# Kernel optimization log

Measured on AMD Instinct MI355X. Metric: run time of the kernel, lower is better.

## Reference

```python
import jax, jax.numpy as jnp
import numpy as np

N_NODES = 50000
N_EDGES = 1600000
D_IN = 128
D_HID = 128
D_OUT = 128


def setup_inputs() -> dict:
    key = jax.random.key(0)
    k1, k2, k3, k4, k5, k6 = jax.random.split(key, 6)
    x = jax.random.normal(k1, (N_NODES, D_IN), dtype=jnp.float32)
    edge_index = jax.random.randint(k2, (2, N_EDGES), 0, N_NODES, dtype=jnp.int64)
    # glorot-ish init for GCNConv linear weights; bias zeros-like but randomized small
    W1 = jax.random.normal(k3, (D_IN, D_HID), dtype=jnp.float32) * (1.0 / np.sqrt(D_IN))
    b1 = jax.random.normal(k4, (D_HID,), dtype=jnp.float32) * 0.01
    W2 = jax.random.normal(k5, (D_HID, D_OUT), dtype=jnp.float32) * (1.0 / np.sqrt(D_HID))
    b2 = jax.random.normal(k6, (D_OUT,), dtype=jnp.float32) * 0.01
    return {"x": x, "edge_index": edge_index, "W1": W1, "b1": b1, "W2": W2, "b2": b2}


def gcn_conv(x, src, dst, W, b, n_nodes):
    # PyG GCNConv: add self-loops, symmetric normalization deg^-1/2, lin -> aggregate -> +bias
    loop = jnp.arange(n_nodes, dtype=src.dtype)
    s = jnp.concatenate([src, loop])  # [E+N]
    d = jnp.concatenate([dst, loop])  # [E+N]
    deg = jax.ops.segment_sum(jnp.ones_like(d, dtype=x.dtype), d, num_segments=n_nodes)
    dinv = jnp.where(deg > 0, jax.lax.rsqrt(deg), 0.0)
    norm = dinv[s] * dinv[d]  # [E+N]
    h = x @ W  # [N, F_out]
    msg = h[s] * norm[:, None]  # gather + scale: [E+N, F_out]
    out = jax.ops.segment_sum(msg, d, num_segments=n_nodes)  # scatter-add
    return out + b


def reference(x, edge_index, W1, b1, W2, b2):
    src, dst = edge_index[0], edge_index[1]
    h = gcn_conv(x, src, dst, W1, b1, N_NODES)
    h = jnp.where(h >= 0, h, 0.1 * h)  # LeakyReLU(0.1)
    h = gcn_conv(h, src, dst, W2, b2, N_NODES)
    return h.mean(axis=1)  # [N]
```

## Files before the change

kernel.cpp:

```cpp
#include <hip/hip_runtime.h>
#include <hip/hip_bf16.h>


#define N_NODES 50000
#define NPAD 50048
#define D 128
#define BK 196
#define CHUNK 4096

typedef unsigned int uint;
typedef unsigned short u16;
typedef __attribute__((ext_vector_type(8))) short short8;
typedef __attribute__((ext_vector_type(4))) float floatx4;

__device__ __forceinline__ u16 cvt_bf16(float f) {
    uint u = __float_as_uint(f);
    return (u16)((u + 0x7fffu + ((u >> 16) & 1u)) >> 16);
}
__device__ __forceinline__ uint pack_bf2(float a, float b) {
    return (uint)cvt_bf16(a) | ((uint)cvt_bf16(b) << 16);
}

__global__ void hist_w2m_kernel(const int* __restrict__ dst, uint* __restrict__ H,
                                const float* __restrict__ W2, const float* __restrict__ b2,
                                float* __restrict__ w2m, uint* __restrict__ counter,
                                int E, int CHN) {
    int t = threadIdx.x, c = blockIdx.x;
    if (c < CHN) {
        __shared__ uint h[BK];
        if (t < BK) h[t] = 0;
        __syncthreads();
        int e0 = c * CHUNK;
        for (int i = t; i < CHUNK; i += 256) {
            int e = e0 + i;
            if (e < E) atomicAdd(&h[dst[e] >> 8], 1u);
        }
        __syncthreads();
        if (t < BK) H[t * CHN + c] = h[t];
    } else {
        if (t < 128) {
            float s = 0.f;
            for (int j = 0; j < 128; j++) s += W2[t * 128 + j];
            w2m[t] = s * (1.0f / 128.0f);
        } else if (t == 128) {
            float s = 0.f;
            for (int j = 0; j < 128; j++) s += b2[j];
            w2m[128] = s * (1.0f / 128.0f);
        } else if (t == 129) {
            *counter = 0;
        }
    }
}

__global__ void scan_kernel(uint* __restrict__ H, uint* __restrict__ T, uint* __restrict__ B,
                            int* __restrict__ row, uint* __restrict__ counter,
                            int CHN, int E, int N) {
    __shared__ uint s[256];
    __shared__ uint ticket_sh;
    int t = threadIdx.x, b = blockIdx.x;
    uint carry = 0;
    for (int base = 0; base < CHN; base += 256) {
        int idx = base + t;
        uint v = (idx < CHN) ? H[b * CHN + idx] : 0u;
        s[t] = v;
        __syncthreads();
#pragma unroll
        for (int off = 1; off < 256; off <<= 1) {
            uint u = (t >= off) ? s[t - off] : 0u;
            __syncthreads();
            s[t] += u;
            __syncthreads();
        }
        if (idx < CHN) H[b * CHN + idx] = carry + s[t] - v;
        carry += s[255];
        __syncthreads();
    }
    if (t == 0) {
        atomicExch(&T[b], carry);
        __threadfence();
        ticket_sh = atomicAdd(counter, 1);
    }
    __syncthreads();
    if (ticket_sh == (uint)(gridDim.x - 1)) {
        __threadfence();
        uint v = (t < BK) ? atomicAdd(&T[t], 0u) : 0u;
        s[t] = v;
        __syncthreads();
#pragma unroll
        for (int off = 1; off < 256; off <<= 1) {
            uint u = (t >= off) ? s[t - off] : 0u;
            __syncthreads();
            s[t] += u;
            __syncthreads();
        }
        if (t < BK) B[t] = s[t] - v;
        if (t == 0) { B[BK] = (uint)E; row[N] = E; }
    }
}

__global__ void scatter_kernel(const int* __restrict__ src, const int* __restrict__ dst,
                               const uint* __restrict__ H, const uint* __restrict__ B,
                               uint* __restrict__ EB, int E, int CHN) {
    __shared__ uint cur[BK];
    int t = threadIdx.x, c = blockIdx.x;
    if (t < BK) cur[t] = B[t] + H[t * CHN + c];
    __syncthreads();
    int e0 = c * CHUNK;
    for (int i = t; i < CHUNK; i += 256) {
        int e = e0 + i;
        if (e < E) {
            int d = dst[e];
            uint slot = atomicAdd(&cur[d >> 8], 1u);
            EB[slot] = ((uint)(d & 255) << 16) | (uint)src[e];
        }
    }
}

#define WT_STRIDE 136
union SortGemmSmem {
    struct { uint cnt[256], s[256], cur[256]; } sort;
    u16 wt[128 * WT_STRIDE];
};
__global__ __launch_bounds__(256) void sortgemm_kernel(
    const uint* __restrict__ EB, const uint* __restrict__ B,
    int* __restrict__ row, float* __restrict__ dinv, u16* __restrict__ esrc,
    const float* __restrict__ A, const float* __restrict__ W,
    uint* __restrict__ G32, int N, int M) {
    __shared__ SortGemmSmem sm;
    int t = threadIdx.x;

    if (blockIdx.x < BK) {
        int b = blockIdx.x;
        uint base = B[b], ne = B[b + 1] - base;
        sm.sort.cnt[t] = 0;
        __syncthreads();
        for (uint i = t; i < ne; i += 256) atomicAdd(&sm.sort.cnt[EB[base + i] >> 16], 1u);
        __syncthreads();
        uint c = sm.sort.cnt[t];
        sm.sort.s[t] = c;
        __syncthreads();
#pragma unroll
        for (int off = 1; off < 256; off <<= 1) {
            uint u = (t >= off) ? sm.sort.s[t - off] : 0u;
            __syncthreads();
            sm.sort.s[t] += u;
            __syncthreads();
        }
        uint p = sm.sort.s[t] - c;
        int v = (b << 8) + t;
        if (v < N) {
            row[v] = (int)(base + p);
            dinv[v] = rsqrtf((float)(c + 1u));
        }
        sm.sort.cur[t] = base + p;
        __syncthreads();
        for (uint i = t; i < ne; i += 256) {
            uint u = EB[base + i];
            uint slot = atomicAdd(&sm.sort.cur[u >> 16], 1u);
            esrc[slot] = (u16)(u & 0xffffu);
        }
    } else {
        int bid = blockIdx.x - BK;
        for (int i = t; i < 128 * 128; i += 256) {
            int k = i >> 7, n = i & 127;
            sm.wt[n * WT_STRIDE + k] = cvt_bf16(W[i]);
        }
        __syncthreads();

        int wave = t >> 6, lane = t & 63;
        int m = lane & 15, quad = lane >> 4;
        int rowa = bid * 64 + wave * 16 + m;
        int rowc = rowa < M ? rowa : M - 1;
        const float* Arow = A + (long)rowc * D;

        short8 afrag[4];
#pragma unroll
        for (int kt = 0; kt < 4; kt++) {
            int k0 = kt * 32 + quad * 8;
            float4 f0 = *(const float4*)(Arow + k0);
            float4 f1 = *(const float4*)(Arow + k0 + 4);
            short8 af;
            af[0] = (short)cvt_bf16(f0.x); af[1] = (short)cvt_bf16(f0.y);
            af[2] = (short)cvt_bf16(f0.z); af[3] = (short)cvt_bf16(f0.w);
            af[4] = (short)cvt_bf16(f1.x); af[5] = (short)cvt_bf16(f1.y);
            af[6] = (short)cvt_bf16(f1.z); af[7] = (short)cvt_bf16(f1.w);
            afrag[kt] = af;
        }

        int orow0 = bid * 64 + wave * 16;
        for (int n0 = 0; n0 < 128; n0 += 16) {
            floatx4 acc = {0.f, 0.f, 0.f, 0.f};
#pragma unroll
            for (int kt = 0; kt < 4; kt++) {
                short8 bf = *(const short8*)(sm.wt + (n0 + m) * WT_STRIDE + kt * 32 + quad * 8);
                acc = __builtin_amdgcn_mfma_f32_16x16x32_bf16(afrag[kt], bf, acc, 0, 0, 0);
            }
#pragma unroll
            for (int r = 0; r < 4; r++) {
                float val = acc[r];
                float oth = __shfl_xor(val, 1, 64);
                int orow = orow0 + quad * 4 + r;
                if (orow < M && (m & 1) == 0)
                    G32[(long)orow * 64 + ((n0 + m) >> 1)] = pack_bf2(val, oth);
            }
        }
    }
}

__global__ __launch_bounds__(256) void gather_node_kernel(
    const int* __restrict__ row, const u16* __restrict__ esrc,
    const uint* __restrict__ g16, const float* __restrict__ dinv,
    const float* __restrict__ b1, const float* __restrict__ w2m,
    float* __restrict__ mg, int N) {
    int wave = threadIdx.x >> 6;
    int lane = threadIdx.x & 63;
    int sub = lane & 7;
    int nb = lane >> 3;
    int v = blockIdx.x * 4 + wave;
    if (v >= N) return;

    const uint4* gv = (const uint4*)g16;
    float dvv = dinv[v];
    float acc[16];
#pragma unroll
    for (int i = 0; i < 16; i++) acc[i] = 0.f;

#define ACC8(ua, ub, wgt) {                                              \
    uint uu[8] = {(ua).x, (ua).y, (ua).z, (ua).w, (ub).x, (ub).y, (ub).z, (ub).w}; \
    _Pragma("unroll")                                                    \
    for (int i = 0; i < 8; i++) {                                        \
        acc[2*i]   += (wgt) * __uint_as_float(uu[i] << 16);              \
        acc[2*i+1] += (wgt) * __uint_as_float(uu[i] & 0xffff0000u);      \
    } }

    if (nb == 0) {
        long rb = (long)v * 16 + 2 * sub;
        uint4 ua = gv[rb], ub = gv[rb + 1];
        ACC8(ua, ub, dvv)
    }
    int jb = row[v], je = row[v + 1];
    int j = jb + nb;
    if (j < je) {
        int s0 = esrc[j];
        float wA = dinv[s0];
        long r0 = (long)s0 * 16 + 2 * sub;
        uint4 p0 = gv[r0], p1 = gv[r0 + 1];
        j += 8;
        while (j < je) {
            int s1 = esrc[j];
            float wB = dinv[s1];
            long r1 = (long)s1 * 16 + 2 * sub;
            uint4 q0 = gv[r1], q1 = gv[r1 + 1];
            j += 8;
            ACC8(p0, p1, wA)
            p0 = q0; p1 = q1; wA = wB;
        }
        ACC8(p0, p1, wA)
    }
#undef ACC8

#pragma unroll
    for (int i = 0; i < 16; i++) {
        acc[i] += __shfl_xor(acc[i], 8, 64);
        acc[i] += __shfl_xor(acc[i], 16, 64);
        acc[i] += __shfl_xor(acc[i], 32, 64);
    }

    if (nb == 0) {
        const float4* bp = (const float4*)b1;
        const float4* wp = (const float4*)w2m;
        float s = 0.f;
#pragma unroll
        for (int q4 = 0; q4 < 4; q4++) {
            float4 bb = bp[sub * 4 + q4];
            float4 wm = wp[sub * 4 + q4];
            float t0 = dvv * acc[4*q4 + 0] + bb.x; t0 = t0 >= 0.f ? t0 : 0.1f * t0;
            float t1 = dvv * acc[4*q4 + 1] + bb.y; t1 = t1 >= 0.f ? t1 : 0.1f * t1;
            float t2 = dvv * acc[4*q4 + 2] + bb.z; t2 = t2 >= 0.f ? t2 : 0.1f * t2;
            float t3 = dvv * acc[4*q4 + 3] + bb.w; t3 = t3 >= 0.f ? t3 : 0.1f * t3;
            s += t0 * wm.x + t1 * wm.y + t2 * wm.z + t3 * wm.w;
        }
        s += __shfl_xor(s, 1, 64);
        s += __shfl_xor(s, 2, 64);
        s += __shfl_xor(s, 4, 64);
        if (sub == 0) mg[v] = dvv * s;
    }
}

__global__ void out_kernel(const int* __restrict__ row, const u16* __restrict__ esrc,
                           const float* __restrict__ mg, const float* __restrict__ dinv,
                           const float* __restrict__ w2m, float* __restrict__ out, int N) {
    int v = blockIdx.x * blockDim.x + threadIdx.x;
    if (v >= N) return;
    float acc = mg[v];
    int jb = row[v], je = row[v + 1];
    int j = jb;
    for (; j + 8 <= je; j += 8) {
        acc += mg[esrc[j]] + mg[esrc[j + 1]] + mg[esrc[j + 2]] + mg[esrc[j + 3]] +
               mg[esrc[j + 4]] + mg[esrc[j + 5]] + mg[esrc[j + 6]] + mg[esrc[j + 7]];
    }
    for (; j < je; j++) acc += mg[esrc[j]];
    out[v] = dinv[v] * acc + w2m[128];
}

extern "C" void kernel_launch(void* const* d_in, const int* in_sizes, int n_in,
                              void* d_out, int out_size, void* d_ws, size_t ws_size,
                              hipStream_t stream) {
    const float* x  = (const float*)d_in[0];
    const int* ei   = (const int*)d_in[1];
    const float* W1 = (const float*)d_in[2];
    const float* b1 = (const float*)d_in[3];
    const float* W2 = (const float*)d_in[4];
    const float* b2 = (const float*)d_in[5];
    float* out = (float*)d_out;

    const int N = N_NODES;
    const int E = in_sizes[1] / 2;
    const int* src = ei;
    const int* dst = ei + E;
    const int CHN = (E + CHUNK - 1) / CHUNK;
    const int nblocks = (N + 255) / 256;

    float*    dinv    = (float*)d_ws;
    int*      row     = (int*)(dinv + NPAD);
    uint*     B       = (uint*)(row + NPAD + 16);
    float*    w2m     = (float*)(B + 256);
    float*    mg      = w2m + 256;
    uint*     T       = (uint*)(mg + NPAD);
    uint*     counter = T + 256;
    uint*     g16u    = counter + 16;
    u16*      esrc    = (u16*)(g16u + (long)NPAD * 64);
    uint*     H       = (uint*)(esrc + E);
    uint*     EB      = H + BK * CHN;

    hist_w2m_kernel<<<CHN + 1, 256, 0, stream>>>(dst, H, W2, b2, w2m, counter, E, CHN);
    scan_kernel<<<BK, 256, 0, stream>>>(H, T, B, row, counter, CHN, E, N);
    scatter_kernel<<<CHN, 256, 0, stream>>>(src, dst, H, B, EB, E, CHN);
    sortgemm_kernel<<<BK + (N + 63) / 64, 256, 0, stream>>>(EB, B, row, dinv, esrc,
                                                            x, W1, g16u, N, N);
    gather_node_kernel<<<(N + 3) / 4, 256, 0, stream>>>(row, esrc, g16u, dinv, b1, w2m, mg, N);
    out_kernel<<<nblocks, 256, 0, stream>>>(row, esrc, mg, dinv, w2m, out, N);
}
```

Baseline: 197.8 us.

## Merge six kernels into three using cooperative grid syncs

Collapses the pipeline from six launches to three. The GEMM moves into the histogram kernel so it can overlap with counting. Scan, scatter and per-bucket sort become one cooperative kernel separated by grid.sync, and the gather and output passes become one persistent cooperative kernel. The aim is to cut launch gaps and tail idle time between small stages, at the cost of grid-wide barriers, a persistent loop with capped occupancy, and a dependence on cooperative launch limits (grid sizes 391 and up to 2048 blocks).

```diff
diff --git a/kernel.cpp b/kernel.cpp
--- a/kernel.cpp
+++ b/kernel.cpp
@@ -1,5 +1,8 @@
 #include <hip/hip_runtime.h>
 #include <hip/hip_bf16.h>
+#include <hip/hip_cooperative_groups.h>
+
+namespace cg = cooperative_groups;
 
 
 #define N_NODES 50000
@@ -7,6 +10,7 @@
 #define D 128
 #define BK 196
 #define CHUNK 4096
+#define WT_STRIDE 136
 
 typedef unsigned int uint;
 typedef unsigned short u16;
@@ -21,23 +25,29 @@
     return (uint)cvt_bf16(a) | ((uint)cvt_bf16(b) << 16);
 }
 
-__global__ void hist_w2m_kernel(const int* __restrict__ dst, uint* __restrict__ H,
-                                const float* __restrict__ W2, const float* __restrict__ b2,
-                                float* __restrict__ w2m, uint* __restrict__ counter,
-                                int E, int CHN) {
+__global__ __launch_bounds__(256) void hist_w2m_gemm_kernel(
+    const int* __restrict__ dst, uint* __restrict__ H,
+    const float* __restrict__ W2, const float* __restrict__ b2,
+    float* __restrict__ w2m,
+    const float* __restrict__ A, const float* __restrict__ W,
+    uint* __restrict__ G32, int E, int CHN, int N) {
+    __shared__ union {
+        uint h[BK];
+        u16 wt[128 * WT_STRIDE];
+    } sm;
     int t = threadIdx.x, c = blockIdx.x;
+
     if (c < CHN) {
-        __shared__ uint h[BK];
-        if (t < BK) h[t] = 0;
+        if (t < BK) sm.h[t] = 0;
         __syncthreads();
         int e0 = c * CHUNK;
         for (int i = t; i < CHUNK; i += 256) {
             int e = e0 + i;
-            if (e < E) atomicAdd(&h[dst[e] >> 8], 1u);
-        }
-        __syncthreads();
-        if (t < BK) H[t * CHN + c] = h[t];
-    } else {
+            if (e < E) atomicAdd(&sm.h[dst[e] >> 8], 1u);
+        }
+        __syncthreads();
+        if (t < BK) H[t * CHN + c] = sm.h[t];
+    } else if (c == CHN) {
         if (t < 128) {
             float s = 0.f;
             for (int j = 0; j < 128; j++) s += W2[t * 128 + j];
@@ -46,121 +56,9 @@
             float s = 0.f;
             for (int j = 0; j < 128; j++) s += b2[j];
             w2m[128] = s * (1.0f / 128.0f);
-        } else if (t == 129) {
-            *counter = 0;
-        }
-    }
-}
-
-__global__ void scan_kernel(uint* __restrict__ H, uint* __restrict__ T, uint* __restrict__ B,
-                            int* __restrict__ row, uint* __restrict__ counter,
-                            int CHN, int E, int N) {
-    __shared__ uint s[256];
-    __shared__ uint ticket_sh;
-    int t = threadIdx.x, b = blockIdx.x;
-    uint carry = 0;
-    for (int base = 0; base < CHN; base += 256) {
-        int idx = base + t;
-        uint v = (idx < CHN) ? H[b * CHN + idx] : 0u;
-        s[t] = v;
-        __syncthreads();
-#pragma unroll
-        for (int off = 1; off < 256; off <<= 1) {
-            uint u = (t >= off) ? s[t - off] : 0u;
-            __syncthreads();
-            s[t] += u;
-            __syncthreads();
-        }
-        if (idx < CHN) H[b * CHN + idx] = carry + s[t] - v;
-        carry += s[255];
-        __syncthreads();
-    }
-    if (t == 0) {
-        atomicExch(&T[b], carry);
-        __threadfence();
-        ticket_sh = atomicAdd(counter, 1);
-    }
-    __syncthreads();
-    if (ticket_sh == (uint)(gridDim.x - 1)) {
-        __threadfence();
-        uint v = (t < BK) ? atomicAdd(&T[t], 0u) : 0u;
-        s[t] = v;
-        __syncthreads();
-#pragma unroll
-        for (int off = 1; off < 256; off <<= 1) {
-            uint u = (t >= off) ? s[t - off] : 0u;
-            __syncthreads();
-            s[t] += u;
-            __syncthreads();
-        }
-        if (t < BK) B[t] = s[t] - v;
-        if (t == 0) { B[BK] = (uint)E; row[N] = E; }
-    }
-}
-
-__global__ void scatter_kernel(const int* __restrict__ src, const int* __restrict__ dst,
-                               const uint* __restrict__ H, const uint* __restrict__ B,
-                               uint* __restrict__ EB, int E, int CHN) {
-    __shared__ uint cur[BK];
-    int t = threadIdx.x, c = blockIdx.x;
-    if (t < BK) cur[t] = B[t] + H[t * CHN + c];
-    __syncthreads();
-    int e0 = c * CHUNK;
-    for (int i = t; i < CHUNK; i += 256) {
-        int e = e0 + i;
-        if (e < E) {
-            int d = dst[e];
-            uint slot = atomicAdd(&cur[d >> 8], 1u);
-            EB[slot] = ((uint)(d & 255) << 16) | (uint)src[e];
-        }
-    }
-}
-
-#define WT_STRIDE 136
-union SortGemmSmem {
-    struct { uint cnt[256], s[256], cur[256]; } sort;
-    u16 wt[128 * WT_STRIDE];
-};
-__global__ __launch_bounds__(256) void sortgemm_kernel(
-    const uint* __restrict__ EB, const uint* __restrict__ B,
-    int* __restrict__ row, float* __restrict__ dinv, u16* __restrict__ esrc,
-    const float* __restrict__ A, const float* __restrict__ W,
-    uint* __restrict__ G32, int N, int M) {
-    __shared__ SortGemmSmem sm;
-    int t = threadIdx.x;
-
-    if (blockIdx.x < BK) {
-        int b = blockIdx.x;
-        uint base = B[b], ne = B[b + 1] - base;
-        sm.sort.cnt[t] = 0;
-        __syncthreads();
-        for (uint i = t; i < ne; i += 256) atomicAdd(&sm.sort.cnt[EB[base + i] >> 16], 1u);
-        __syncthreads();
-        uint c = sm.sort.cnt[t];
-        sm.sort.s[t] = c;
-        __syncthreads();
-#pragma unroll
-        for (int off = 1; off < 256; off <<= 1) {
-            uint u = (t >= off) ? sm.sort.s[t - off] : 0u;
-            __syncthreads();
-            sm.sort.s[t] += u;
-            __syncthreads();
-        }
-        uint p = sm.sort.s[t] - c;
-        int v = (b << 8) + t;
-        if (v < N) {
-            row[v] = (int)(base + p);
-            dinv[v] = rsqrtf((float)(c + 1u));
-        }
-        sm.sort.cur[t] = base + p;
-        __syncthreads();
-        for (uint i = t; i < ne; i += 256) {
-            uint u = EB[base + i];
-            uint slot = atomicAdd(&sm.sort.cur[u >> 16], 1u);
-            esrc[slot] = (u16)(u & 0xffffu);
         }
     } else {
-        int bid = blockIdx.x - BK;
+        int bid = c - CHN - 1;
         for (int i = t; i < 128 * 128; i += 256) {
             int k = i >> 7, n = i & 127;
             sm.wt[n * WT_STRIDE + k] = cvt_bf16(W[i]);
@@ -170,7 +68,7 @@
         int wave = t >> 6, lane = t & 63;
         int m = lane & 15, quad = lane >> 4;
         int rowa = bid * 64 + wave * 16 + m;
-        int rowc = rowa < M ? rowa : M - 1;
+        int rowc = rowa < N ? rowa : N - 1;
         const float* Arow = A + (long)rowc * D;
 
         short8 afrag[4];
@@ -200,30 +98,122 @@
                 float val = acc[r];
                 float oth = __shfl_xor(val, 1, 64);
                 int orow = orow0 + quad * 4 + r;
-                if (orow < M && (m & 1) == 0)
+                if (orow < N && (m & 1) == 0)
                     G32[(long)orow * 64 + ((n0 + m) >> 1)] = pack_bf2(val, oth);
             }
         }
     }
 }
 
-__global__ __launch_bounds__(256) void gather_node_kernel(
+__global__ __launch_bounds__(256) void build_kernel(
+    const int* __restrict__ src, const int* __restrict__ dst,
+    uint* __restrict__ H, uint* __restrict__ T, uint* __restrict__ B,
+    int* __restrict__ row, float* __restrict__ dinv, u16* __restrict__ esrc,
+    uint* __restrict__ EB, int E, int N, int CHN) {
+    cg::grid_group grid = cg::this_grid();
+    __shared__ union {
+        uint s[256];
+        struct { uint cnt[256]; uint s2[256]; uint cur2[256]; } srt;
+        uint cur[BK];
+    } sm;
+    int t = threadIdx.x, b = blockIdx.x;
+
+    if (b < BK) {
+        uint carry = 0;
+        for (int base = 0; base < CHN; base += 256) {
+            int idx = base + t;
+            uint v = (idx < CHN) ? H[b * CHN + idx] : 0u;
+            sm.s[t] = v;
+            __syncthreads();
+#pragma unroll
+            for (int off = 1; off < 256; off <<= 1) {
+                uint u = (t >= off) ? sm.s[t - off] : 0u;
+                __syncthreads();
+                sm.s[t] += u;
+                __syncthreads();
+            }
+            if (idx < CHN) H[b * CHN + idx] = carry + sm.s[t] - v;
+            carry += sm.s[255];
+            __syncthreads();
+        }
+        if (t == 0) atomicExch(&T[b], carry);
+    }
+    grid.sync();
+
+    if (b == 0) {
+        uint v = (t < BK) ? atomicAdd(&T[t], 0u) : 0u;
+        sm.s[t] = v;
+        __syncthreads();
+#pragma unroll
+        for (int off = 1; off < 256; off <<= 1) {
+            uint u = (t >= off) ? sm.s[t - off] : 0u;
+            __syncthreads();
+            sm.s[t] += u;
+            __syncthreads();
+        }
+        if (t < BK) B[t] = sm.s[t] - v;
+        if (t == 0) { B[BK] = (uint)E; row[N] = E; }
+    }
+    grid.sync();
+
+    if (b < CHN) {
+        if (t < BK) sm.cur[t] = B[t] + H[t * CHN + b];
+        __syncthreads();
+        int e0 = b * CHUNK;
+        for (int i = t; i < CHUNK; i += 256) {
+            int e = e0 + i;
+            if (e < E) {
+                int d = dst[e];
+                uint slot = atomicAdd(&sm.cur[d >> 8], 1u);
+                EB[slot] = ((uint)(d & 255) << 16) | (uint)src[e];
+            }
+        }
+    }
+    grid.sync();
+
+    if (b < BK) {
+        uint base = B[b], ne = B[b + 1] - base;
+        sm.srt.cnt[t] = 0;
+        __syncthreads();
+        for (uint i = t; i < ne; i += 256) atomicAdd(&sm.srt.cnt[EB[base + i] >> 16], 1u);
+        __syncthreads();
+        uint cval = sm.srt.cnt[t];
+        sm.srt.s2[t] = cval;
+        __syncthreads();
+#pragma unroll
+        for (int off = 1; off < 256; off <<= 1) {
+            uint u = (t >= off) ? sm.srt.s2[t - off] : 0u;
+            __syncthreads();
+            sm.srt.s2[t] += u;
+            __syncthreads();
+        }
+        uint p = sm.srt.s2[t] - cval;
+        int v = (b << 8) + t;
+        if (v < N) {
+            row[v] = (int)(base + p);
+            dinv[v] = rsqrtf((float)(cval + 1u));
+        }
+        sm.srt.cur2[t] = base + p;
+        __syncthreads();
+        for (uint i = t; i < ne; i += 256) {
+            uint u = EB[base + i];
+            uint slot = atomicAdd(&sm.srt.cur2[u >> 16], 1u);
+            esrc[slot] = (u16)(u & 0xffffu);
+        }
+    }
+}
+
+__global__ __launch_bounds__(256, 8) void gather_out_kernel(
     const int* __restrict__ row, const u16* __restrict__ esrc,
     const uint* __restrict__ g16, const float* __restrict__ dinv,
     const float* __restrict__ b1, const float* __restrict__ w2m,
-    float* __restrict__ mg, int N) {
+    float* __restrict__ mg, float* __restrict__ out, int N) {
+    cg::grid_group grid = cg::this_grid();
     int wave = threadIdx.x >> 6;
     int lane = threadIdx.x & 63;
     int sub = lane & 7;
     int nb = lane >> 3;
-    int v = blockIdx.x * 4 + wave;
-    if (v >= N) return;
-
     const uint4* gv = (const uint4*)g16;
-    float dvv = dinv[v];
-    float acc[16];
-#pragma unroll
-    for (int i = 0; i < 16; i++) acc[i] = 0.f;
 
 #define ACC8(ua, ub, wgt) {                                              \
     uint uu[8] = {(ua).x, (ua).y, (ua).z, (ua).w, (ub).x, (ub).y, (ub).z, (ub).w}; \
@@ -233,74 +223,83 @@
         acc[2*i+1] += (wgt) * __uint_as_float(uu[i] & 0xffff0000u);      \
     } }
 
-    if (nb == 0) {
-        long rb = (long)v * 16 + 2 * sub;
-        uint4 ua = gv[rb], ub = gv[rb + 1];
-        ACC8(ua, ub, dvv)
-    }
-    int jb = row[v], je = row[v + 1];
-    int j = jb + nb;
-    if (j < je) {
-        int s0 = esrc[j];
-        float wA = dinv[s0];
-        long r0 = (long)s0 * 16 + 2 * sub;
-        uint4 p0 = gv[r0], p1 = gv[r0 + 1];
-        j += 8;
-        while (j < je) {
-            int s1 = esrc[j];
-            float wB = dinv[s1];
-            long r1 = (long)s1 * 16 + 2 * sub;
-            uint4 q0 = gv[r1], q1 = gv[r1 + 1];
-            j += 8;
-            ACC8(p0, p1, wA)
-            p0 = q0; p1 = q1; wA = wB;
-        }
-        ACC8(p0, p1, wA)
+    for (int v0 = blockIdx.x * 4; v0 < N; v0 += gridDim.x * 4) {
+        int v = v0 + wave;
+        if (v < N) {
+            float dvv = dinv[v];
+            float acc[16];
+#pragma unroll
+            for (int i = 0; i < 16; i++) acc[i] = 0.f;
+
+            if (nb == 0) {
+                long rb = (long)v * 16 + 2 * sub;
+                uint4 ua = gv[rb], ub = gv[rb + 1];
+                ACC8(ua, ub, dvv)
+            }
+            int jb = row[v], je = row[v + 1];
+            int j = jb + nb;
+            if (j < je) {
+                int s0 = esrc[j];
+                float wA = dinv[s0];
+                long r0 = (long)s0 * 16 + 2 * sub;
+                uint4 p0 = gv[r0], p1 = gv[r0 + 1];
+                j += 8;
+                while (j < je) {
+                    int s1 = esrc[j];
+                    float wB = dinv[s1];
+                    long r1 = (long)s1 * 16 + 2 * sub;
+                    uint4 q0 = gv[r1], q1 = gv[r1 + 1];
+                    j += 8;
+                    ACC8(p0, p1, wA)
+                    p0 = q0; p1 = q1; wA = wB;
+                }
+                ACC8(p0, p1, wA)
+            }
+
+#pragma unroll
+            for (int i = 0; i < 16; i++) {
+                acc[i] += __shfl_xor(acc[i], 8, 64);
+                acc[i] += __shfl_xor(acc[i], 16, 64);
+                acc[i] += __shfl_xor(acc[i], 32, 64);
+            }
+
+            if (nb == 0) {
+                const float4* bp = (const float4*)b1;
+                const float4* wp = (const float4*)w2m;
+                float s = 0.f;
+#pragma unroll
+                for (int q4 = 0; q4 < 4; q4++) {
+                    float4 bb = bp[sub * 4 + q4];
+                    float4 wm = wp[sub * 4 + q4];
+                    float t0 = dvv * acc[4*q4 + 0] + bb.x; t0 = t0 >= 0.f ? t0 : 0.1f * t0;
+                    float t1 = dvv * acc[4*q4 + 1] + bb.y; t1 = t1 >= 0.f ? t1 : 0.1f * t1;
+                    float t2 = dvv * acc[4*q4 + 2] + bb.z; t2 = t2 >= 0.f ? t2 : 0.1f * t2;
+                    float t3 = dvv * acc[4*q4 + 3] + bb.w; t3 = t3 >= 0.f ? t3 : 0.1f * t3;
+                    s += t0 * wm.x + t1 * wm.y + t2 * wm.z + t3 * wm.w;
+                }
+                s += __shfl_xor(s, 1, 64);
+                s += __shfl_xor(s, 2, 64);
+                s += __shfl_xor(s, 4, 64);
+                if (sub == 0) mg[v] = dvv * s;
+            }
+        }
     }
 #undef ACC8
 
-#pragma unroll
-    for (int i = 0; i < 16; i++) {
-        acc[i] += __shfl_xor(acc[i], 8, 64);
-        acc[i] += __shfl_xor(acc[i], 16, 64);
-        acc[i] += __shfl_xor(acc[i], 32, 64);
-    }
-
-    if (nb == 0) {
-        const float4* bp = (const float4*)b1;
-        const float4* wp = (const float4*)w2m;
-        float s = 0.f;
-#pragma unroll
-        for (int q4 = 0; q4 < 4; q4++) {
-            float4 bb = bp[sub * 4 + q4];
-            float4 wm = wp[sub * 4 + q4];
-            float t0 = dvv * acc[4*q4 + 0] + bb.x; t0 = t0 >= 0.f ? t0 : 0.1f * t0;
-            float t1 = dvv * acc[4*q4 + 1] + bb.y; t1 = t1 >= 0.f ? t1 : 0.1f * t1;
-            float t2 = dvv * acc[4*q4 + 2] + bb.z; t2 = t2 >= 0.f ? t2 : 0.1f * t2;
-            float t3 = dvv * acc[4*q4 + 3] + bb.w; t3 = t3 >= 0.f ? t3 : 0.1f * t3;
-            s += t0 * wm.x + t1 * wm.y + t2 * wm.z + t3 * wm.w;
-        }
-        s += __shfl_xor(s, 1, 64);
-        s += __shfl_xor(s, 2, 64);
-        s += __shfl_xor(s, 4, 64);
-        if (sub == 0) mg[v] = dvv * s;
-    }
-}
-
-__global__ void out_kernel(const int* __restrict__ row, const u16* __restrict__ esrc,
-                           const float* __restrict__ mg, const float* __restrict__ dinv,
-                           const float* __restrict__ w2m, float* __restrict__ out, int N) {
-    int v = blockIdx.x * blockDim.x + threadIdx.x;
-    if (v >= N) return;
-    float acc = mg[v];
-    int jb = row[v], je = row[v + 1];
-    int j = jb;
-    for (; j + 8 <= je; j += 8) {
-        acc += mg[esrc[j]] + mg[esrc[j + 1]] + mg[esrc[j + 2]] + mg[esrc[j + 3]] +
-               mg[esrc[j + 4]] + mg[esrc[j + 5]] + mg[esrc[j + 6]] + mg[esrc[j + 7]];
-    }
-    for (; j < je; j++) acc += mg[esrc[j]];
-    out[v] = dinv[v] * acc + w2m[128];
+    grid.sync();
+
+    float w2c = w2m[128];
+    for (int v = blockIdx.x * 256 + threadIdx.x; v < N; v += gridDim.x * 256) {
+        float acc = mg[v];
+        int jb = row[v], je = row[v + 1];
+        int j = jb;
+        for (; j + 8 <= je; j += 8) {
+            acc += mg[esrc[j]] + mg[esrc[j + 1]] + mg[esrc[j + 2]] + mg[esrc[j + 3]] +
+                   mg[esrc[j + 4]] + mg[esrc[j + 5]] + mg[esrc[j + 6]] + mg[esrc[j + 7]];
+        }
+        for (; j < je; j++) acc += mg[esrc[j]];
+        out[v] = dinv[v] * acc + w2c;
+    }
 }
 
 extern "C" void kernel_launch(void* const* d_in, const int* in_sizes, int n_in,
@@ -314,12 +313,12 @@
     const float* b2 = (const float*)d_in[5];
     float* out = (float*)d_out;
 
-    const int N = N_NODES;
-    const int E = in_sizes[1] / 2;
+    int N = N_NODES;
+    int E = in_sizes[1] / 2;
     const int* src = ei;
     const int* dst = ei + E;
-    const int CHN = (E + CHUNK - 1) / CHUNK;
-    const int nblocks = (N + 255) / 256;
+    int CHN = (E + CHUNK - 1) / CHUNK;
+    int GB  = (N + 63) / 64;
 
     float*    dinv    = (float*)d_ws;
     int*      row     = (int*)(dinv + NPAD);
@@ -332,12 +331,36 @@
     u16*      esrc    = (u16*)(g16u + (long)NPAD * 64);
     uint*     H       = (uint*)(esrc + E);
     uint*     EB      = H + BK * CHN;
-
-    hist_w2m_kernel<<<CHN + 1, 256, 0, stream>>>(dst, H, W2, b2, w2m, counter, E, CHN);
-    scan_kernel<<<BK, 256, 0, stream>>>(H, T, B, row, counter, CHN, E, N);
-    scatter_kernel<<<CHN, 256, 0, stream>>>(src, dst, H, B, EB, E, CHN);
-    sortgemm_kernel<<<BK + (N + 63) / 64, 256, 0, stream>>>(EB, B, row, dinv, esrc,
-                                                            x, W1, g16u, N, N);
-    gather_node_kernel<<<(N + 3) / 4, 256, 0, stream>>>(row, esrc, g16u, dinv, b1, w2m, mg, N);
-    out_kernel<<<nblocks, 256, 0, stream>>>(row, esrc, mg, dinv, w2m, out, N);
-}
+    (void)counter;
+
+    hist_w2m_gemm_kernel<<<CHN + 1 + GB, 256, 0, stream>>>(dst, H, W2, b2, w2m,
+                                                           x, W1, g16u, E, CHN, N);
+
+    {
+        int grid2 = (CHN > BK) ? CHN : BK;
+        void* args[] = {(void*)&src, (void*)&dst, (void*)&H, (void*)&T, (void*)&B,
+                        (void*)&row, (void*)&dinv, (void*)&esrc, (void*)&EB,
+                        (void*)&E, (void*)&N, (void*)&CHN};
+        hipLaunchCooperativeKernel((const void*)build_kernel, dim3(grid2), dim3(256),
+                                   args, 0, stream);
+    }
+
+    {
+        static int maxb = -1;
+        if (maxb < 0) {
+            int mb = 0;
+            if (hipOccupancyMaxActiveBlocksPerMultiprocessor(
+                    &mb, (const void*)gather_out_kernel, 256, 0) != hipSuccess || mb < 1)
+                mb = 4;
+            maxb = mb;
+        }
+        int grid3 = maxb * 256;
+        int ng = (N + 3) / 4;
+        if (grid3 > ng) grid3 = ng;
+        if (grid3 > 2048) grid3 = 2048;
+        void* args[] = {(void*)&row, (void*)&esrc, (void*)&g16u, (void*)&dinv,
+                        (void*)&b1, (void*)&w2m, (void*)&mg, (void*)&out, (void*)&N};
+        hipLaunchCooperativeKernel((const void*)gather_out_kernel, dim3(grid3), dim3(256),
+                                   args, 0, stream);
+    }
+}
```

New measurement: 495.4 us. 2.5x slower.

## Replace two-level bucket sort with global-atomic degree count and fused scan

Applied to the files above, without the earlier changes.

Replaces the bucketed histogram, scan, scatter and local sort kernels with a per-node global atomic degree count, a scan that runs in the same launch and waits on spin counters, and a direct scatter via per-node global atomic cursors. This cuts the launch count from six to four plus a memset and removes the intermediate EB buffer and its second pass. The cost is heavy global atomic contention on 50k counters and inter-block spin waits, which can deadlock if the counting blocks are not scheduled before the waiting scan blocks. Edge order within a node also becomes nondeterministic.

```diff
diff --git a/kernel.cpp b/kernel.cpp
--- a/kernel.cpp
+++ b/kernel.cpp
@@ -5,8 +5,8 @@
 #define N_NODES 50000
 #define NPAD 50048
 #define D 128
-#define BK 196
 #define CHUNK 4096
+#define WT_STRIDE 136
 
 typedef unsigned int uint;
 typedef unsigned short u16;
@@ -21,23 +21,25 @@
     return (uint)cvt_bf16(a) | ((uint)cvt_bf16(b) << 16);
 }
 
-__global__ void hist_w2m_kernel(const int* __restrict__ dst, uint* __restrict__ H,
-                                const float* __restrict__ W2, const float* __restrict__ b2,
-                                float* __restrict__ w2m, uint* __restrict__ counter,
-                                int E, int CHN) {
+__global__ __launch_bounds__(256) void degscan_kernel(
+    const int* __restrict__ dst, const float* __restrict__ W2,
+    const float* __restrict__ b2, float* __restrict__ w2m,
+    int* __restrict__ row, uint* __restrict__ cnt, uint* __restrict__ T,
+    float* __restrict__ dinv, uint* __restrict__ cur,
+    int E, int CHN, int N) {
     int t = threadIdx.x, c = blockIdx.x;
+    uint* rowu = (uint*)row;
+
     if (c < CHN) {
-        __shared__ uint h[BK];
-        if (t < BK) h[t] = 0;
-        __syncthreads();
         int e0 = c * CHUNK;
         for (int i = t; i < CHUNK; i += 256) {
             int e = e0 + i;
-            if (e < E) atomicAdd(&h[dst[e] >> 8], 1u);
-        }
-        __syncthreads();
-        if (t < BK) H[t * CHN + c] = h[t];
-    } else {
+            if (e < E) atomicAdd(&rowu[dst[e]], 1u);
+        }
+        __threadfence();
+        __syncthreads();
+        if (t == 0) atomicAdd(&cnt[0], 1u);
+    } else if (c == CHN) {
         if (t < 128) {
             float s = 0.f;
             for (int j = 0; j < 128; j++) s += W2[t * 128 + j];
@@ -46,23 +48,19 @@
             float s = 0.f;
             for (int j = 0; j < 128; j++) s += b2[j];
             w2m[128] = s * (1.0f / 128.0f);
-        } else if (t == 129) {
-            *counter = 0;
-        }
-    }
-}
-
-__global__ void scan_kernel(uint* __restrict__ H, uint* __restrict__ T, uint* __restrict__ B,
-                            int* __restrict__ row, uint* __restrict__ counter,
-                            int CHN, int E, int N) {
-    __shared__ uint s[256];
-    __shared__ uint ticket_sh;
-    int t = threadIdx.x, b = blockIdx.x;
-    uint carry = 0;
-    for (int base = 0; base < CHN; base += 256) {
-        int idx = base + t;
-        uint v = (idx < CHN) ? H[b * CHN + idx] : 0u;
-        s[t] = v;
+        }
+    } else {
+        __shared__ uint s[256];
+        __shared__ uint Bb_sh;
+        int NSB = (int)gridDim.x - CHN - 1;
+        int b = c - CHN - 1;
+        if (t == 0) {
+            while (atomicAdd(&cnt[0], 0u) < (uint)CHN) __builtin_amdgcn_s_sleep(8);
+        }
+        __syncthreads();
+        int v = b * 256 + t;
+        uint cv = (v < N) ? atomicAdd(&rowu[v], 0u) : 0u;
+        s[t] = cv;
         __syncthreads();
 #pragma unroll
         for (int off = 1; off < 256; off <<= 1) {
@@ -71,20 +69,16 @@
             s[t] += u;
             __syncthreads();
         }
-        if (idx < CHN) H[b * CHN + idx] = carry + s[t] - v;
-        carry += s[255];
-        __syncthreads();
-    }
-    if (t == 0) {
-        atomicExch(&T[b], carry);
-        __threadfence();
-        ticket_sh = atomicAdd(counter, 1);
-    }
-    __syncthreads();
-    if (ticket_sh == (uint)(gridDim.x - 1)) {
-        __threadfence();
-        uint v = (t < BK) ? atomicAdd(&T[t], 0u) : 0u;
-        s[t] = v;
+        uint excl = s[t] - cv;
+        if (t == 0) {
+            atomicExch(&T[b], s[255]);
+            __threadfence();
+            atomicAdd(&cnt[1], 1u);
+            while (atomicAdd(&cnt[1], 0u) < (uint)NSB) __builtin_amdgcn_s_sleep(8);
+        }
+        __syncthreads();
+        uint tv = (t < NSB) ? atomicAdd(&T[t], 0u) : 0u;
+        s[t] = tv;
         __syncthreads();
 #pragma unroll
         for (int off = 1; off < 256; off <<= 1) {
@@ -93,77 +87,42 @@
             s[t] += u;
             __syncthreads();
         }
-        if (t < BK) B[t] = s[t] - v;
-        if (t == 0) { B[BK] = (uint)E; row[N] = E; }
-    }
-}
-
-__global__ void scatter_kernel(const int* __restrict__ src, const int* __restrict__ dst,
-                               const uint* __restrict__ H, const uint* __restrict__ B,
-                               uint* __restrict__ EB, int E, int CHN) {
-    __shared__ uint cur[BK];
-    int t = threadIdx.x, c = blockIdx.x;
-    if (t < BK) cur[t] = B[t] + H[t * CHN + c];
-    __syncthreads();
-    int e0 = c * CHUNK;
-    for (int i = t; i < CHUNK; i += 256) {
-        int e = e0 + i;
-        if (e < E) {
-            int d = dst[e];
-            uint slot = atomicAdd(&cur[d >> 8], 1u);
-            EB[slot] = ((uint)(d & 255) << 16) | (uint)src[e];
-        }
-    }
-}
-
-#define WT_STRIDE 136
-union SortGemmSmem {
-    struct { uint cnt[256], s[256], cur[256]; } sort;
-    u16 wt[128 * WT_STRIDE];
-};
-__global__ __launch_bounds__(256) void sortgemm_kernel(
-    const uint* __restrict__ EB, const uint* __restrict__ B,
-    int* __restrict__ row, float* __restrict__ dinv, u16* __restrict__ esrc,
+        if (t == b) Bb_sh = s[t] - tv;
+        __syncthreads();
+        uint base = Bb_sh;
+        if (v < N) {
+            uint r = base + excl;
+            row[v] = (int)r;
+            cur[v] = r;
+            dinv[v] = rsqrtf((float)(cv + 1u));
+        }
+        if (b == 0 && t == 0) row[N] = E;
+    }
+}
+
+__global__ __launch_bounds__(256) void scattergemm_kernel(
+    const int* __restrict__ src, const int* __restrict__ dst,
+    uint* __restrict__ cur, u16* __restrict__ esrc,
     const float* __restrict__ A, const float* __restrict__ W,
-    uint* __restrict__ G32, int N, int M) {
-    __shared__ SortGemmSmem sm;
+    uint* __restrict__ G32, int E, int CHN, int M) {
+    __shared__ u16 wt[128 * WT_STRIDE];
     int t = threadIdx.x;
 
-    if (blockIdx.x < BK) {
-        int b = blockIdx.x;
-        uint base = B[b], ne = B[b + 1] - base;
-        sm.sort.cnt[t] = 0;
-        __syncthreads();
-        for (uint i = t; i < ne; i += 256) atomicAdd(&sm.sort.cnt[EB[base + i] >> 16], 1u);
-        __syncthreads();
-        uint c = sm.sort.cnt[t];
-        sm.sort.s[t] = c;
-        __syncthreads();
-#pragma unroll
-        for (int off = 1; off < 256; off <<= 1) {
-            uint u = (t >= off) ? sm.sort.s[t - off] : 0u;
-            __syncthreads();
-            sm.sort.s[t] += u;
-            __syncthreads();
-        }
-        uint p = sm.sort.s[t] - c;
-        int v = (b << 8) + t;
-        if (v < N) {
-            row[v] = (int)(base + p);
-            dinv[v] = rsqrtf((float)(c + 1u));
-        }
-        sm.sort.cur[t] = base + p;
-        __syncthreads();
-        for (uint i = t; i < ne; i += 256) {
-            uint u = EB[base + i];
-            uint slot = atomicAdd(&sm.sort.cur[u >> 16], 1u);
-            esrc[slot] = (u16)(u & 0xffffu);
+    if (blockIdx.x < (uint)CHN) {
+        int e0 = blockIdx.x * CHUNK;
+        for (int i = t; i < CHUNK; i += 256) {
+            int e = e0 + i;
+            if (e < E) {
+                int d = dst[e];
+                uint slot = atomicAdd(&cur[d], 1u);
+                esrc[slot] = (u16)src[e];
+            }
         }
     } else {
-        int bid = blockIdx.x - BK;
+        int bid = blockIdx.x - CHN;
         for (int i = t; i < 128 * 128; i += 256) {
             int k = i >> 7, n = i & 127;
-            sm.wt[n * WT_STRIDE + k] = cvt_bf16(W[i]);
+            wt[n * WT_STRIDE + k] = cvt_bf16(W[i]);
         }
         __syncthreads();
 
@@ -192,7 +151,7 @@
             floatx4 acc = {0.f, 0.f, 0.f, 0.f};
 #pragma unroll
             for (int kt = 0; kt < 4; kt++) {
-                short8 bf = *(const short8*)(sm.wt + (n0 + m) * WT_STRIDE + kt * 32 + quad * 8);
+                short8 bf = *(const short8*)(wt + (n0 + m) * WT_STRIDE + kt * 32 + quad * 8);
                 acc = __builtin_amdgcn_mfma_f32_16x16x32_bf16(afrag[kt], bf, acc, 0, 0, 0);
             }
 #pragma unroll
@@ -319,25 +278,25 @@
     const int* src = ei;
     const int* dst = ei + E;
     const int CHN = (E + CHUNK - 1) / CHUNK;
-    const int nblocks = (N + 255) / 256;
-
-    float*    dinv    = (float*)d_ws;
-    int*      row     = (int*)(dinv + NPAD);
-    uint*     B       = (uint*)(row + NPAD + 16);
-    float*    w2m     = (float*)(B + 256);
-    float*    mg      = w2m + 256;
-    uint*     T       = (uint*)(mg + NPAD);
-    uint*     counter = T + 256;
-    uint*     g16u    = counter + 16;
-    u16*      esrc    = (u16*)(g16u + (long)NPAD * 64);
-    uint*     H       = (uint*)(esrc + E);
-    uint*     EB      = H + BK * CHN;
-
-    hist_w2m_kernel<<<CHN + 1, 256, 0, stream>>>(dst, H, W2, b2, w2m, counter, E, CHN);
-    scan_kernel<<<BK, 256, 0, stream>>>(H, T, B, row, counter, CHN, E, N);
-    scatter_kernel<<<CHN, 256, 0, stream>>>(src, dst, H, B, EB, E, CHN);
-    sortgemm_kernel<<<BK + (N + 63) / 64, 256, 0, stream>>>(EB, B, row, dinv, esrc,
-                                                            x, W1, g16u, N, N);
+    const int NSB = (N + 255) / 256;
+    const int GB  = (N + 63) / 64;
+
+    float*    dinv = (float*)d_ws;
+    int*      row  = (int*)(dinv + NPAD);
+    uint*     cnt  = (uint*)(row + NPAD);
+    uint*     T    = (uint*)(row + NPAD + 16);
+    float*    w2m  = (float*)(T + 256);
+    float*    mg   = w2m + 256;
+    uint*     cur  = (uint*)(mg + NPAD);
+    uint*     g16u = cur + NPAD;
+    u16*      esrc = (u16*)(g16u + (long)NPAD * 64);
+
+    hipMemsetAsync(row, 0, (size_t)(NPAD + 2) * sizeof(int), stream);
+
+    degscan_kernel<<<CHN + 1 + NSB, 256, 0, stream>>>(dst, W2, b2, w2m,
+                                                      row, cnt, T, dinv, cur, E, CHN, N);
+    scattergemm_kernel<<<CHN + GB, 256, 0, stream>>>(src, dst, cur, esrc,
+                                                     x, W1, g16u, E, CHN, N);
     gather_node_kernel<<<(N + 3) / 4, 256, 0, stream>>>(row, esrc, g16u, dinv, b1, w2m, mg, N);
-    out_kernel<<<nblocks, 256, 0, stream>>>(row, esrc, mg, dinv, w2m, out, N);
-}
+    out_kernel<<<NSB, 256, 0, stream>>>(row, esrc, mg, dinv, w2m, out, N);
+}
```

Measured after the change: 366.0 us. 1.85x slower.

## Batch neighbor index loads via wave shuffles and double GEMM rows per block

Applied to the files above, without the earlier changes.

The gather kernel now loads up to 64 neighbor indices and their dinv weights with one coalesced load per wave, then broadcasts them to the 8-lane subgroups with shuffles. This replaces the serial per-subgroup index and weight loads that sat on the dependent path. The fused GEMM branch now processes two 64-row groups per block, halving the GEMM block count and the cost of loading and converting W into shared memory. The trade-off is more shuffles and higher register pressure.

```diff
diff --git a/kernel.cpp b/kernel.cpp
--- a/kernel.cpp
+++ b/kernel.cpp
@@ -169,39 +169,43 @@
 
         int wave = t >> 6, lane = t & 63;
         int m = lane & 15, quad = lane >> 4;
-        int rowa = bid * 64 + wave * 16 + m;
-        int rowc = rowa < M ? rowa : M - 1;
-        const float* Arow = A + (long)rowc * D;
-
-        short8 afrag[4];
-#pragma unroll
-        for (int kt = 0; kt < 4; kt++) {
-            int k0 = kt * 32 + quad * 8;
-            float4 f0 = *(const float4*)(Arow + k0);
-            float4 f1 = *(const float4*)(Arow + k0 + 4);
-            short8 af;
-            af[0] = (short)cvt_bf16(f0.x); af[1] = (short)cvt_bf16(f0.y);
-            af[2] = (short)cvt_bf16(f0.z); af[3] = (short)cvt_bf16(f0.w);
-            af[4] = (short)cvt_bf16(f1.x); af[5] = (short)cvt_bf16(f1.y);
-            af[6] = (short)cvt_bf16(f1.z); af[7] = (short)cvt_bf16(f1.w);
-            afrag[kt] = af;
-        }
-
-        int orow0 = bid * 64 + wave * 16;
-        for (int n0 = 0; n0 < 128; n0 += 16) {
-            floatx4 acc = {0.f, 0.f, 0.f, 0.f};
+
+#pragma unroll
+        for (int rg = 0; rg < 2; rg++) {
+            int rowa = bid * 128 + rg * 64 + wave * 16 + m;
+            int rowc = rowa < M ? rowa : M - 1;
+            const float* Arow = A + (long)rowc * D;
+
+            short8 afrag[4];
 #pragma unroll
             for (int kt = 0; kt < 4; kt++) {
-                short8 bf = *(const short8*)(sm.wt + (n0 + m) * WT_STRIDE + kt * 32 + quad * 8);
-                acc = __builtin_amdgcn_mfma_f32_16x16x32_bf16(afrag[kt], bf, acc, 0, 0, 0);
+                int k0 = kt * 32 + quad * 8;
+                float4 f0 = *(const float4*)(Arow + k0);
+                float4 f1 = *(const float4*)(Arow + k0 + 4);
+                short8 af;
+                af[0] = (short)cvt_bf16(f0.x); af[1] = (short)cvt_bf16(f0.y);
+                af[2] = (short)cvt_bf16(f0.z); af[3] = (short)cvt_bf16(f0.w);
+                af[4] = (short)cvt_bf16(f1.x); af[5] = (short)cvt_bf16(f1.y);
+                af[6] = (short)cvt_bf16(f1.z); af[7] = (short)cvt_bf16(f1.w);
+                afrag[kt] = af;
             }
-#pragma unroll
-            for (int r = 0; r < 4; r++) {
-                float val = acc[r];
-                float oth = __shfl_xor(val, 1, 64);
-                int orow = orow0 + quad * 4 + r;
-                if (orow < M && (m & 1) == 0)
-                    G32[(long)orow * 64 + ((n0 + m) >> 1)] = pack_bf2(val, oth);
+
+            int orow0 = bid * 128 + rg * 64 + wave * 16;
+            for (int n0 = 0; n0 < 128; n0 += 16) {
+                floatx4 acc = {0.f, 0.f, 0.f, 0.f};
+#pragma unroll
+                for (int kt = 0; kt < 4; kt++) {
+                    short8 bf = *(const short8*)(sm.wt + (n0 + m) * WT_STRIDE + kt * 32 + quad * 8);
+                    acc = __builtin_amdgcn_mfma_f32_16x16x32_bf16(afrag[kt], bf, acc, 0, 0, 0);
+                }
+#pragma unroll
+                for (int r = 0; r < 4; r++) {
+                    float val = acc[r];
+                    float oth = __shfl_xor(val, 1, 64);
+                    int orow = orow0 + quad * 4 + r;
+                    if (orow < M && (m & 1) == 0)
+                        G32[(long)orow * 64 + ((n0 + m) >> 1)] = pack_bf2(val, oth);
+                }
             }
         }
     }
@@ -239,23 +243,46 @@
         ACC8(ua, ub, dvv)
     }
     int jb = row[v], je = row[v + 1];
-    int j = jb + nb;
-    if (j < je) {
-        int s0 = esrc[j];
-        float wA = dinv[s0];
-        long r0 = (long)s0 * 16 + 2 * sub;
-        uint4 p0 = gv[r0], p1 = gv[r0 + 1];
-        j += 8;
-        while (j < je) {
-            int s1 = esrc[j];
-            float wB = dinv[s1];
-            long r1 = (long)s1 * 16 + 2 * sub;
-            uint4 q0 = gv[r1], q1 = gv[r1 + 1];
-            j += 8;
+    for (int base = jb; base < je; base += 64) {
+        int navail = je - base; if (navail > 64) navail = 64;
+        int mi = 0; float mw = 0.f;
+        if (lane < navail) {
+            mi = (int)esrc[base + lane];
+            mw = dinv[mi];
+        }
+        int sk0, sk1, sk2, sk3, sk4, sk5, sk6, sk7;
+        float wk0, wk1, wk2, wk3, wk4, wk5, wk6, wk7;
+        sk0 = __shfl(mi, nb,      64); wk0 = __shfl(mw, nb,      64);
+        sk1 = __shfl(mi, nb + 8,  64); wk1 = __shfl(mw, nb + 8,  64);
+        sk2 = __shfl(mi, nb + 16, 64); wk2 = __shfl(mw, nb + 16, 64);
+        sk3 = __shfl(mi, nb + 24, 64); wk3 = __shfl(mw, nb + 24, 64);
+        sk4 = __shfl(mi, nb + 32, 64); wk4 = __shfl(mw, nb + 32, 64);
+        sk5 = __shfl(mi, nb + 40, 64); wk5 = __shfl(mw, nb + 40, 64);
+        sk6 = __shfl(mi, nb + 48, 64); wk6 = __shfl(mw, nb + 48, 64);
+        sk7 = __shfl(mi, nb + 56, 64); wk7 = __shfl(mw, nb + 56, 64);
+        int kmax = (navail > nb) ? ((navail - nb + 7) >> 3) : 0;
+
+        if (kmax > 0) {
+            long rA = (long)sk0 * 16 + 2 * sub;
+            uint4 p0 = gv[rA], p1 = gv[rA + 1];
+            float wA = wk0;
+#define SLOT(kk, skk, wkk) \
+            if (kk < kmax) { \
+                long rB = (long)(skk) * 16 + 2 * sub; \
+                uint4 q0 = gv[rB], q1 = gv[rB + 1]; \
+                ACC8(p0, p1, wA) \
+                p0 = q0; p1 = q1; wA = (wkk); \
+            }
+            SLOT(1, sk1, wk1)
+            SLOT(2, sk2, wk2)
+            SLOT(3, sk3, wk3)
+            SLOT(4, sk4, wk4)
+            SLOT(5, sk5, wk5)
+            SLOT(6, sk6, wk6)
+            SLOT(7, sk7, wk7)
+#undef SLOT
             ACC8(p0, p1, wA)
-            p0 = q0; p1 = q1; wA = wB;
-        }
-        ACC8(p0, p1, wA)
+        }
     }
 #undef ACC8
 
@@ -320,6 +347,7 @@
     const int* dst = ei + E;
     const int CHN = (E + CHUNK - 1) / CHUNK;
     const int nblocks = (N + 255) / 256;
+    const int GB = (N + 127) / 128;
 
     float*    dinv    = (float*)d_ws;
     int*      row     = (int*)(dinv + NPAD);
@@ -336,8 +364,8 @@
     hist_w2m_kernel<<<CHN + 1, 256, 0, stream>>>(dst, H, W2, b2, w2m, counter, E, CHN);
     scan_kernel<<<BK, 256, 0, stream>>>(H, T, B, row, counter, CHN, E, N);
     scatter_kernel<<<CHN, 256, 0, stream>>>(src, dst, H, B, EB, E, CHN);
-    sortgemm_kernel<<<BK + (N + 63) / 64, 256, 0, stream>>>(EB, B, row, dinv, esrc,
-                                                            x, W1, g16u, N, N);
+    sortgemm_kernel<<<BK + GB, 256, 0, stream>>>(EB, B, row, dinv, esrc,
+                                                 x, W1, g16u, N, N);
     gather_node_kernel<<<(N + 3) / 4, 256, 0, stream>>>(row, esrc, g16u, dinv, b1, w2m, mg, N);
     out_kernel<<<nblocks, 256, 0, stream>>>(row, esrc, mg, dinv, w2m, out, N);
 }
```

Result: slower. 201.9 us (+2.1%).
